# Kernel tuning notes

Measured on AMD Instinct MI355X. Metric: run time of the kernel, lower is better.

The kernel has to match this reference:

```python
import jax, jax.numpy as jnp
import numpy as np

NEG_SLOPE = 0.01  # torch.nn.LeakyReLU default


def setup_inputs() -> dict:
    key = jax.random.key(0)
    k1, k2, k3 = jax.random.split(key, 3)
    B, T, U, H, O = 8, 300, 80, 512, 640
    input_TN = jax.random.normal(k1, (B, T, 1, H), dtype=jnp.float32)
    input_PN = jax.random.normal(k2, (B, 1, U, H), dtype=jnp.float32)
    # joint_network: Linear(input_size=2H, n_neurons=O)
    W = jax.random.normal(k3, (2 * H, O), dtype=jnp.float32) / np.sqrt(2 * H)
    b = jnp.zeros((O,), dtype=jnp.float32)
    return {"input_TN": input_TN, "input_PN": input_PN, "W": W, "b": b}


def reference(input_TN, input_PN, W, b):
    # joint == "concat": expand TN/PN to (B,T,U,H), concat on last dim -> (B,T,U,2H),
    # then Linear, then LeakyReLU. Mathematically, Linear(cat(x, y)) ==
    # x @ W[:H] + y @ W[H:] + b, which avoids materializing the (B,T,U,2H) tensor.
    H = input_TN.shape[-1]
    Wt, Wp = W[:H], W[H:]
    tn_proj = jnp.einsum("btuh,ho->btuo", input_TN, Wt)  # (B,T,1,O)
    pn_proj = jnp.einsum("btuh,ho->btuo", input_PN, Wp)  # (B,1,U,O)
    joint = tn_proj + pn_proj + b                         # (B,T,U,O)
    return jax.nn.leaky_relu(joint, negative_slope=NEG_SLOPE)
```

## Files before the change

### kernel.cpp

```cpp
#include <hip/hip_runtime.h>


#define DIM_H 512
#define DIM_O 640
#define DIM_B 8
#define DIM_T 300
#define DIM_U 80
#define M_TN  2400
#define M_PN  640
#define NEG_SLOPE 0.01f

#define BK 16
#define NB_N (DIM_O / 64)
#define NB_TN (((M_TN + 63) / 64) * NB_N)
#define NB_PN (((M_PN + 63) / 64) * NB_N)

__global__ __launch_bounds__(256, 2) void proj_gemm(
    const float* __restrict__ tn_in,
    const float* __restrict__ pn_in,
    const float* __restrict__ W,
    const float* __restrict__ bias,
    float* __restrict__ tn_out,
    float* __restrict__ pn_out)
{
    const int bid = blockIdx.x;
    const float* A; const float* Wp; float* Cout; int M; bool addb; int local;
    if (bid < NB_TN) {
        A = tn_in; Wp = W;               Cout = tn_out; M = M_TN; addb = false; local = bid;
    } else {
        A = pn_in; Wp = W + DIM_H * DIM_O; Cout = pn_out; M = M_PN; addb = true;  local = bid - NB_TN;
    }
    const int bm = local / NB_N;
    const int bn = local - bm * NB_N;
    const int row0 = bm * 64;
    const int col0 = bn * 64;

    __shared__ float As[BK][68];
    __shared__ float Bs[BK][64];

    const int tid = threadIdx.x;
    const int ty = tid >> 4;
    const int tx = tid & 15;
    const int ar  = tid >> 2;
    const int ac4 = (tid & 3) << 2;
    const int br  = tid >> 4;
    const int bc4 = (tid & 15) << 2;

    float acc[4][4];
    #pragma unroll
    for (int i = 0; i < 4; ++i)
        #pragma unroll
        for (int j = 0; j < 4; ++j) acc[i][j] = 0.f;

    const int gr = row0 + ar;
    for (int k0 = 0; k0 < DIM_H; k0 += BK) {
        float4 av = make_float4(0.f, 0.f, 0.f, 0.f);
        if (gr < M) av = *(const float4*)(A + (size_t)gr * DIM_H + k0 + ac4);
        const float4 bv = *(const float4*)(Wp + (size_t)(k0 + br) * DIM_O + col0 + bc4);

        __syncthreads();
        As[ac4 + 0][ar] = av.x;
        As[ac4 + 1][ar] = av.y;
        As[ac4 + 2][ar] = av.z;
        As[ac4 + 3][ar] = av.w;
        *(float4*)&Bs[br][bc4] = bv;
        __syncthreads();

        #pragma unroll
        for (int kk = 0; kk < BK; ++kk) {
            const float4 a = *(const float4*)&As[kk][ty << 2];
            const float4 b = *(const float4*)&Bs[kk][tx << 2];
            acc[0][0] = fmaf(a.x, b.x, acc[0][0]);
            acc[0][1] = fmaf(a.x, b.y, acc[0][1]);
            acc[0][2] = fmaf(a.x, b.z, acc[0][2]);
            acc[0][3] = fmaf(a.x, b.w, acc[0][3]);
            acc[1][0] = fmaf(a.y, b.x, acc[1][0]);
            acc[1][1] = fmaf(a.y, b.y, acc[1][1]);
            acc[1][2] = fmaf(a.y, b.z, acc[1][2]);
            acc[1][3] = fmaf(a.y, b.w, acc[1][3]);
            acc[2][0] = fmaf(a.z, b.x, acc[2][0]);
            acc[2][1] = fmaf(a.z, b.y, acc[2][1]);
            acc[2][2] = fmaf(a.z, b.z, acc[2][2]);
            acc[2][3] = fmaf(a.z, b.w, acc[2][3]);
            acc[3][0] = fmaf(a.w, b.x, acc[3][0]);
            acc[3][1] = fmaf(a.w, b.y, acc[3][1]);
            acc[3][2] = fmaf(a.w, b.z, acc[3][2]);
            acc[3][3] = fmaf(a.w, b.w, acc[3][3]);
        }
    }

    float4 bsv = make_float4(0.f, 0.f, 0.f, 0.f);
    if (addb) bsv = *(const float4*)(bias + col0 + (tx << 2));
    #pragma unroll
    for (int i = 0; i < 4; ++i) {
        const int r = row0 + (ty << 2) + i;
        if (r < M) {
            float4 v;
            v.x = acc[i][0] + bsv.x;
            v.y = acc[i][1] + bsv.y;
            v.z = acc[i][2] + bsv.z;
            v.w = acc[i][3] + bsv.w;
            *(float4*)(Cout + (size_t)r * DIM_O + col0 + (tx << 2)) = v;
        }
    }
}

__global__ __launch_bounds__(256) void joint_kernel(
    const float* __restrict__ tn_proj,
    const float* __restrict__ pn_proj,
    float* __restrict__ out)
{
    const int bt = blockIdx.x;
    const int b = bt / DIM_T;
    const int tid = threadIdx.x;

    __shared__ float4 tns[DIM_O / 4];
    if (tid < DIM_O / 4)
        tns[tid] = ((const float4*)(tn_proj + (size_t)bt * DIM_O))[tid];
    __syncthreads();

    const float4* __restrict__ pn4 = (const float4*)(pn_proj + (size_t)b * DIM_U * DIM_O);
    float4* __restrict__ out4 = (float4*)(out + (size_t)bt * DIM_U * DIM_O);

    const int total = DIM_U * (DIM_O / 4);
    for (int idx = tid; idx < total; idx += 256) {
        const int u = idx / (DIM_O / 4);
        const int o4 = idx - u * (DIM_O / 4);
        const float4 t = tns[o4];
        const float4 p = pn4[idx];
        float4 r;
        r.x = t.x + p.x;
        r.y = t.y + p.y;
        r.z = t.z + p.z;
        r.w = t.w + p.w;
        r.x = fmaxf(r.x, 0.f) + NEG_SLOPE * fminf(r.x, 0.f);
        r.y = fmaxf(r.y, 0.f) + NEG_SLOPE * fminf(r.y, 0.f);
        r.z = fmaxf(r.z, 0.f) + NEG_SLOPE * fminf(r.z, 0.f);
        r.w = fmaxf(r.w, 0.f) + NEG_SLOPE * fminf(r.w, 0.f);
        out4[idx] = r;
    }
}

extern "C" void kernel_launch(void* const* d_in, const int* in_sizes, int n_in,
                              void* d_out, int out_size, void* d_ws, size_t ws_size,
                              hipStream_t stream) {
    const float* tn   = (const float*)d_in[0];
    const float* pn   = (const float*)d_in[1];
    const float* W    = (const float*)d_in[2];
    const float* bias = (const float*)d_in[3];
    float* out = (float*)d_out;

    float* tn_proj = (float*)d_ws;
    float* pn_proj = tn_proj + (size_t)M_TN * DIM_O;

    proj_gemm<<<NB_TN + NB_PN, 256, 0, stream>>>(tn, pn, W, bias, tn_proj, pn_proj);
    joint_kernel<<<M_TN, 256, 0, stream>>>(tn_proj, pn_proj, out);
}
```

Baseline: 535.3 us.

## Prefetch GEMM tiles into registers, widen BK, and stream joint output with nontemporal stores

The projection GEMM doubles its K tile to 32 and loads the next tile into registers while the current one is being computed, hiding global load latency behind the FMA loop. The joint kernel now runs 640 threads so each thread keeps a fixed o4 column and its tn value in a register, which removes the per-iteration division and shared-memory read. Output writes use nontemporal stores to avoid polluting the cache with the large output. The cost is more registers for the prefetch buffers, and a larger block for the joint kernel.

```diff
diff --git a/kernel.cpp b/kernel.cpp
--- a/kernel.cpp
+++ b/kernel.cpp
@@ -10,10 +10,12 @@
 #define M_PN  640
 #define NEG_SLOPE 0.01f
 
-#define BK 16
+#define BK 32
 #define NB_N (DIM_O / 64)
 #define NB_TN (((M_TN + 63) / 64) * NB_N)
 #define NB_PN (((M_PN + 63) / 64) * NB_N)
+
+typedef float f32x4 __attribute__((ext_vector_type(4)));
 
 __global__ __launch_bounds__(256, 2) void proj_gemm(
     const float* __restrict__ tn_in,
@@ -26,7 +28,7 @@
     const int bid = blockIdx.x;
     const float* A; const float* Wp; float* Cout; int M; bool addb; int local;
     if (bid < NB_TN) {
-        A = tn_in; Wp = W;               Cout = tn_out; M = M_TN; addb = false; local = bid;
+        A = tn_in; Wp = W;                 Cout = tn_out; M = M_TN; addb = false; local = bid;
     } else {
         A = pn_in; Wp = W + DIM_H * DIM_O; Cout = pn_out; M = M_PN; addb = true;  local = bid - NB_TN;
     }
@@ -41,10 +43,10 @@
     const int tid = threadIdx.x;
     const int ty = tid >> 4;
     const int tx = tid & 15;
-    const int ar  = tid >> 2;
-    const int ac4 = (tid & 3) << 2;
-    const int br  = tid >> 4;
-    const int bc4 = (tid & 15) << 2;
+    const int ar = tid >> 2;
+    const int ac = (tid & 3) << 3;
+    const int br = tid >> 3;
+    const int bc = (tid & 7) << 3;
 
     float acc[4][4];
     #pragma unroll
@@ -53,59 +55,68 @@
         for (int j = 0; j < 4; ++j) acc[i][j] = 0.f;
 
     const int gr = row0 + ar;
+    const bool arow_ok = (gr < M);
+    const float* __restrict__ Arow = A + (size_t)gr * DIM_H;
+    const float* __restrict__ Bbase = Wp + col0;
+
+    f32x4 a0 = 0.f, a1 = 0.f, b0, b1;
+    if (arow_ok) {
+        a0 = *(const f32x4*)(Arow + ac);
+        a1 = *(const f32x4*)(Arow + ac + 4);
+    }
+    b0 = *(const f32x4*)(Bbase + (size_t)br * DIM_O + bc);
+    b1 = *(const f32x4*)(Bbase + (size_t)br * DIM_O + bc + 4);
+
     for (int k0 = 0; k0 < DIM_H; k0 += BK) {
-        float4 av = make_float4(0.f, 0.f, 0.f, 0.f);
-        if (gr < M) av = *(const float4*)(A + (size_t)gr * DIM_H + k0 + ac4);
-        const float4 bv = *(const float4*)(Wp + (size_t)(k0 + br) * DIM_O + col0 + bc4);
+        __syncthreads();
+        #pragma unroll
+        for (int j = 0; j < 4; ++j) {
+            As[ac + j][ar]     = a0[j];
+            As[ac + 4 + j][ar] = a1[j];
+        }
+        *(f32x4*)&Bs[br][bc]     = b0;
+        *(f32x4*)&Bs[br][bc + 4] = b1;
+        __syncthreads();
 
-        __syncthreads();
-        As[ac4 + 0][ar] = av.x;
-        As[ac4 + 1][ar] = av.y;
-        As[ac4 + 2][ar] = av.z;
-        As[ac4 + 3][ar] = av.w;
-        *(float4*)&Bs[br][bc4] = bv;
-        __syncthreads();
+        const int kn = k0 + BK;
+        if (kn < DIM_H) {
+            if (arow_ok) {
+                a0 = *(const f32x4*)(Arow + kn + ac);
+                a1 = *(const f32x4*)(Arow + kn + ac + 4);
+            }
+            b0 = *(const f32x4*)(Bbase + (size_t)(kn + br) * DIM_O + bc);
+            b1 = *(const f32x4*)(Bbase + (size_t)(kn + br) * DIM_O + bc + 4);
+        }
 
         #pragma unroll
         for (int kk = 0; kk < BK; ++kk) {
-            const float4 a = *(const float4*)&As[kk][ty << 2];
-            const float4 b = *(const float4*)&Bs[kk][tx << 2];
-            acc[0][0] = fmaf(a.x, b.x, acc[0][0]);
-            acc[0][1] = fmaf(a.x, b.y, acc[0][1]);
-            acc[0][2] = fmaf(a.x, b.z, acc[0][2]);
-            acc[0][3] = fmaf(a.x, b.w, acc[0][3]);
-            acc[1][0] = fmaf(a.y, b.x, acc[1][0]);
-            acc[1][1] = fmaf(a.y, b.y, acc[1][1]);
-            acc[1][2] = fmaf(a.y, b.z, acc[1][2]);
-            acc[1][3] = fmaf(a.y, b.w, acc[1][3]);
-            acc[2][0] = fmaf(a.z, b.x, acc[2][0]);
-            acc[2][1] = fmaf(a.z, b.y, acc[2][1]);
-            acc[2][2] = fmaf(a.z, b.z, acc[2][2]);
-            acc[2][3] = fmaf(a.z, b.w, acc[2][3]);
-            acc[3][0] = fmaf(a.w, b.x, acc[3][0]);
-            acc[3][1] = fmaf(a.w, b.y, acc[3][1]);
-            acc[3][2] = fmaf(a.w, b.z, acc[3][2]);
-            acc[3][3] = fmaf(a.w, b.w, acc[3][3]);
+            const f32x4 a = *(const f32x4*)&As[kk][ty << 2];
+            const f32x4 b = *(const f32x4*)&Bs[kk][tx << 2];
+            #pragma unroll
+            for (int i = 0; i < 4; ++i) {
+                acc[i][0] = fmaf(a[i], b[0], acc[i][0]);
+                acc[i][1] = fmaf(a[i], b[1], acc[i][1]);
+                acc[i][2] = fmaf(a[i], b[2], acc[i][2]);
+                acc[i][3] = fmaf(a[i], b[3], acc[i][3]);
+            }
         }
     }
 
-    float4 bsv = make_float4(0.f, 0.f, 0.f, 0.f);
-    if (addb) bsv = *(const float4*)(bias + col0 + (tx << 2));
+    f32x4 bsv = 0.f;
+    if (addb) bsv = *(const f32x4*)(bias + col0 + (tx << 2));
     #pragma unroll
     for (int i = 0; i < 4; ++i) {
         const int r = row0 + (ty << 2) + i;
         if (r < M) {
-            float4 v;
-            v.x = acc[i][0] + bsv.x;
-            v.y = acc[i][1] + bsv.y;
-            v.z = acc[i][2] + bsv.z;
-            v.w = acc[i][3] + bsv.w;
-            *(float4*)(Cout + (size_t)r * DIM_O + col0 + (tx << 2)) = v;
+            f32x4 v;
+            #pragma unroll
+            for (int j = 0; j < 4; ++j) v[j] = acc[i][j] + bsv[j];
+            *(f32x4*)(Cout + (size_t)r * DIM_O + col0 + (tx << 2)) = v;
         }
     }
 }
 
-__global__ __launch_bounds__(256) void joint_kernel(
+__global__ __launch_bounds__(640) void joint_kernel(
     const float* __restrict__ tn_proj,
     const float* __restrict__ pn_proj,
     float* __restrict__ out)
@@ -114,30 +125,27 @@
     const int b = bt / DIM_T;
     const int tid = threadIdx.x;
 
-    __shared__ float4 tns[DIM_O / 4];
+    __shared__ f32x4 tns[DIM_O / 4];
     if (tid < DIM_O / 4)
-        tns[tid] = ((const float4*)(tn_proj + (size_t)bt * DIM_O))[tid];
+        tns[tid] = ((const f32x4*)(tn_proj + (size_t)bt * DIM_O))[tid];
     __syncthreads();
 
-    const float4* __restrict__ pn4 = (const float4*)(pn_proj + (size_t)b * DIM_U * DIM_O);
-    float4* __restrict__ out4 = (float4*)(out + (size_t)bt * DIM_U * DIM_O);
+    const int o4 = tid % (DIM_O / 4);
+    const f32x4 t = tns[o4];
 
-    const int total = DIM_U * (DIM_O / 4);
-    for (int idx = tid; idx < total; idx += 256) {
-        const int u = idx / (DIM_O / 4);
-        const int o4 = idx - u * (DIM_O / 4);
-        const float4 t = tns[o4];
-        const float4 p = pn4[idx];
-        float4 r;
-        r.x = t.x + p.x;
-        r.y = t.y + p.y;
-        r.z = t.z + p.z;
-        r.w = t.w + p.w;
-        r.x = fmaxf(r.x, 0.f) + NEG_SLOPE * fminf(r.x, 0.f);
-        r.y = fmaxf(r.y, 0.f) + NEG_SLOPE * fminf(r.y, 0.f);
-        r.z = fmaxf(r.z, 0.f) + NEG_SLOPE * fminf(r.z, 0.f);
-        r.w = fmaxf(r.w, 0.f) + NEG_SLOPE * fminf(r.w, 0.f);
-        out4[idx] = r;
+    const f32x4* __restrict__ pn4 = (const f32x4*)(pn_proj + (size_t)b * DIM_U * DIM_O);
+    f32x4* __restrict__ out4 = (f32x4*)(out + (size_t)bt * DIM_U * DIM_O);
+
+    #pragma unroll 4
+    for (int idx = tid; idx < DIM_U * (DIM_O / 4); idx += 640) {
+        const f32x4 p = pn4[idx];
+        f32x4 r;
+        #pragma unroll
+        for (int j = 0; j < 4; ++j) {
+            const float x = t[j] + p[j];
+            r[j] = fmaxf(x, 0.f) + NEG_SLOPE * fminf(x, 0.f);
+        }
+        __builtin_nontemporal_store(r, &out4[idx]);
     }
 }
 
@@ -154,5 +162,5 @@
     float* pn_proj = tn_proj + (size_t)M_TN * DIM_O;
 
     proj_gemm<<<NB_TN + NB_PN, 256, 0, stream>>>(tn, pn, W, bias, tn_proj, pn_proj);
-    joint_kernel<<<M_TN, 256, 0, stream>>>(tn_proj, pn_proj, out);
+    joint_kernel<<<M_TN, 640, 0, stream>>>(tn_proj, pn_proj, out);
 }
```

New measurement: 522.6 us. -2.4%, faster.
